# Kernel optimization log

Measured on AMD Instinct MI355X. Metric: run time of the kernel, lower is better.

The kernel has to match this reference:

```python
import jax, jax.numpy as jnp
import numpy as np

PZ = 16          # partition_size
SMOOTH = 1e-8


def setup_inputs() -> dict:
    key = jax.random.key(0)
    k1, k2, k3, k4 = jax.random.split(key, 4)
    shape = (4, 2, 160, 160, 160)  # [N, C, Z, X, Y]
    pred = jax.random.uniform(k1, shape, dtype=jnp.float32)
    groundtruth = jax.random.uniform(k2, shape, dtype=jnp.float32)
    a = jax.random.uniform(k3, (1,), dtype=jnp.float32)
    b = jax.random.uniform(k4, (1,), dtype=jnp.float32)
    return {"pred": pred, "groundtruth": groundtruth, "a": a, "b": b}


def _blocks(t):
    # [N,C,Z,X,Y] -> rows of per-(block, channel) voxels [N*nz*nx*ny*C, PZ^3]
    # matches the torch loops: blocks ordered (N, zz, xx, yy) with channel dim
    # of each block concatenated along dim 0 before flattening dims 1..-1.
    N, C, Z, X, Y = t.shape
    nz, nx, ny = Z // PZ, X // PZ, Y // PZ
    t = t.reshape(N, C, nz, PZ, nx, PZ, ny, PZ)
    t = t.transpose(0, 2, 4, 6, 1, 3, 5, 7)  # [N,nz,nx,ny,C,pz,pz,pz]
    return t.reshape(N * nz * nx * ny * C, PZ * PZ * PZ)


def reference(pred, groundtruth, a, b):
    p = _blocks(pred)
    g = _blocks(groundtruth)
    tp = jnp.sum(g * p, axis=1)
    fn = jnp.sum(g * (1.0 - p), axis=1)
    fp = jnp.sum((1.0 - g) * p, axis=1)
    denom = fp + fn + SMOOTH
    alpha = a + b * ((fp + SMOOTH) / denom)
    beta = a + b * ((fn + SMOOTH) / denom)
    loss = jnp.sum(1.0 - (tp + SMOOTH) / (tp + alpha * fp + beta * fn + SMOOTH))
    return loss
```

## Files before the change

### kernel.cpp

```cpp
#include <hip/hip_runtime.h>

#define SMOOTH 1e-8f

typedef float f32x4 __attribute__((ext_vector_type(4)));

constexpr int NROWS = 8000;
constexpr int WG1   = 3200;

__global__ __launch_bounds__(256, 4)
void partial_kernel(const float* __restrict__ pred,
                    const float* __restrict__ gt,
                    float* __restrict__ wsq)
{
    int wg = blockIdx.x;
    const int q4 = wg & 3;  wg >>= 2;
    const int c  = wg & 1;  wg >>= 1;
    const int xx = wg % 10; wg /= 10;
    const int zz = wg % 10;
    const int n  = wg / 10;

    const int t    = threadIdx.x;
    const int lane = t & 63;
    const int wave = t >> 6;
    const int z    = zz * 16 + q4 * 4 + wave;

    const long pb = ((long)((n * 2 + c) * 160 + z) * 160 + xx * 16) * 40L;

    const f32x4* p4 = reinterpret_cast<const f32x4*>(pred) + pb + lane;
    const f32x4* g4 = reinterpret_cast<const f32x4*>(gt)  + pb + lane;

    f32x4 P[10], G[10];
    #pragma unroll
    for (int k = 0; k < 10; ++k) {
        P[k] = __builtin_nontemporal_load(p4 + k * 64);
        G[k] = __builtin_nontemporal_load(g4 + k * 64);
    }

    float aS[5] = {0, 0, 0, 0, 0};
    float aG[5] = {0, 0, 0, 0, 0};
    float aP[5] = {0, 0, 0, 0, 0};
    #pragma unroll
    for (int k = 0; k < 10; ++k) {
        const int m = k % 5;
        const f32x4 p = P[k], g = G[k];
        aS[m] += (p.x + p.y) + (p.z + p.w);
        aG[m] += (g.x + g.y) + (g.z + g.w);
        aP[m] += p.x * g.x + p.y * g.y + p.z * g.z + p.w * g.w;
    }

    int rr[5];
    #pragma unroll
    for (int m = 0; m < 5; ++m)
        rr[m] = ((lane + 24 * m) % 40) >> 3;

    float bS[5], bG[5], bP[5];
    #pragma unroll
    for (int r = 0; r < 5; ++r) {
        float s = 0.f, g = 0.f, p = 0.f;
        #pragma unroll
        for (int m = 0; m < 5; ++m) {
            const bool hit = (rr[m] == r);
            s += hit ? aS[m] : 0.f;
            g += hit ? aG[m] : 0.f;
            p += hit ? aP[m] : 0.f;
        }
        bS[r] = s; bG[r] = g; bP[r] = p;
    }

    #pragma unroll
    for (int r = 0; r < 5; ++r) {
        #pragma unroll
        for (int d = 0; d < 5; ++d) {
            const int msk = (d < 2) ? (1 << d) : (1 << (d + 1));
            bS[r] += __shfl_xor(bS[r], msk, 64);
            bG[r] += __shfl_xor(bG[r], msk, 64);
            bP[r] += __shfl_xor(bP[r], msk, 64);
        }
    }

    __shared__ float red[4][2][15];
    const int b = (lane >> 2) & 1;
    if ((lane & 59) == 0) {
        #pragma unroll
        for (int r = 0; r < 5; ++r) {
            red[wave][b][r * 3 + 0] = bS[r];
            red[wave][b][r * 3 + 1] = bG[r];
            red[wave][b][r * 3 + 2] = bP[r];
        }
    }
    __syncthreads();

    if (t < 30) {
        const int yy   = t / 3;
        const int comp = t - yy * 3;
        const int bb = yy & 1, r = yy >> 1;
        const float val = red[0][bb][r * 3 + comp] + red[1][bb][r * 3 + comp] +
                          red[2][bb][r * 3 + comp] + red[3][bb][r * 3 + comp];
        const int row = (((n * 10 + zz) * 10 + xx) * 10 + yy) * 2 + c;
        wsq[(row * 4 + q4) * 3 + comp] = val;
    }
}

__global__ __launch_bounds__(1024)
void finalize_kernel(const float* __restrict__ wsq,
                     const float* __restrict__ a_p,
                     const float* __restrict__ b_p,
                     float* __restrict__ out)
{
    const int t = threadIdx.x;
    const float a = a_p[0], b = b_p[0];
    float sum = 0.f;

    for (int r = t; r < NROWS; r += 1024) {
        const float4 w0 = *reinterpret_cast<const float4*>(wsq + r * 12);
        const float4 w1 = *reinterpret_cast<const float4*>(wsq + r * 12 + 4);
        const float4 w2 = *reinterpret_cast<const float4*>(wsq + r * 12 + 8);
        const float SP  = w0.x + w0.w + w1.z + w2.y;
        const float SG  = w0.y + w1.x + w1.w + w2.z;
        const float SGP = w0.z + w1.y + w2.x + w2.w;

        const float tp = SGP;
        const float fn = SG - SGP;
        const float fp = SP - SGP;
        const float denom = fp + fn + SMOOTH;
        const float alpha = a + b * ((fp + SMOOTH) / denom);
        const float beta  = a + b * ((fn + SMOOTH) / denom);
        sum += 1.f - (tp + SMOOTH) / (tp + alpha * fp + beta * fn + SMOOTH);
    }

    #pragma unroll
    for (int d = 32; d > 0; d >>= 1) sum += __shfl_down(sum, d, 64);

    __shared__ float wsum[16];
    if ((t & 63) == 0) wsum[t >> 6] = sum;
    __syncthreads();
    if (t == 0) {
        float tot = 0.f;
        #pragma unroll
        for (int i = 0; i < 16; ++i) tot += wsum[i];
        out[0] = tot;
    }
}

extern "C" void kernel_launch(void* const* d_in, const int* in_sizes, int n_in,
                              void* d_out, int out_size, void* d_ws, size_t ws_size,
                              hipStream_t stream)
{
    const float* pred = (const float*)d_in[0];
    const float* gt   = (const float*)d_in[1];
    const float* a_p  = (const float*)d_in[2];
    const float* b_p  = (const float*)d_in[3];
    float* out = (float*)d_out;
    float* wsq = (float*)d_ws;

    partial_kernel<<<WG1, 256, 0, stream>>>(pred, gt, wsq);
    finalize_kernel<<<1, 1024, 0, stream>>>(wsq, a_p, b_p, out);
}
```

Before: 252.8 us.

## Use single-wave workgroups with double-buffered plane loads and parallel atomic finalize

Each partial-kernel workgroup becomes one 64-lane wave that processes four z-planes in sequence. It uses two register buffers so the loads for the next plane are issued before the current plane is summed, with sched_barriers to keep that order. This drops the cross-wave LDS reduction and gives each wave more loads in flight. The finalize step now runs across many blocks and combines results with atomicAdd, which needs an extra launch to zero the output. The cost is a launch of only 3200 tiny workgroups, higher register pressure from 40 vector registers of buffers, and an extra kernel launch.

```diff
diff --git a/kernel.cpp b/kernel.cpp
--- a/kernel.cpp
+++ b/kernel.cpp
@@ -7,7 +7,9 @@
 constexpr int NROWS = 8000;
 constexpr int WG1   = 3200;
 
-__global__ __launch_bounds__(256, 4)
+__global__ void zero_out_kernel(float* out) { out[0] = 0.0f; }
+
+__global__ __launch_bounds__(64, 2)
 void partial_kernel(const float* __restrict__ pred,
                     const float* __restrict__ gt,
                     float* __restrict__ wsq)
@@ -19,34 +21,49 @@
     const int zz = wg % 10;
     const int n  = wg / 10;
 
-    const int t    = threadIdx.x;
-    const int lane = t & 63;
-    const int wave = t >> 6;
-    const int z    = zz * 16 + q4 * 4 + wave;
+    const int lane = threadIdx.x;
+    const int z0   = zz * 16 + q4 * 4;
 
-    const long pb = ((long)((n * 2 + c) * 160 + z) * 160 + xx * 16) * 40L;
+    const long pb0 = ((long)((n * 2 + c) * 160 + z0) * 160 + xx * 16) * 40L;
+    constexpr long PSTR = 6400;
 
-    const f32x4* p4 = reinterpret_cast<const f32x4*>(pred) + pb + lane;
-    const f32x4* g4 = reinterpret_cast<const f32x4*>(gt)  + pb + lane;
+    const f32x4* p4 = reinterpret_cast<const f32x4*>(pred) + pb0 + lane;
+    const f32x4* g4 = reinterpret_cast<const f32x4*>(gt)  + pb0 + lane;
 
-    f32x4 P[10], G[10];
-    #pragma unroll
-    for (int k = 0; k < 10; ++k) {
-        P[k] = __builtin_nontemporal_load(p4 + k * 64);
-        G[k] = __builtin_nontemporal_load(g4 + k * 64);
+    f32x4 PA[10], GA[10], PB[10], GB[10];
+    float aS[5] = {0,0,0,0,0}, aG[5] = {0,0,0,0,0}, aP[5] = {0,0,0,0,0};
+
+#define ISSUE(Pbuf, Gbuf, plane)                                              \
+    _Pragma("unroll")                                                         \
+    for (int k = 0; k < 10; ++k) {                                            \
+        Pbuf[k] = __builtin_nontemporal_load(p4 + (plane) * PSTR + k * 64);   \
+        Gbuf[k] = __builtin_nontemporal_load(g4 + (plane) * PSTR + k * 64);   \
     }
 
-    float aS[5] = {0, 0, 0, 0, 0};
-    float aG[5] = {0, 0, 0, 0, 0};
-    float aP[5] = {0, 0, 0, 0, 0};
-    #pragma unroll
-    for (int k = 0; k < 10; ++k) {
-        const int m = k % 5;
-        const f32x4 p = P[k], g = G[k];
-        aS[m] += (p.x + p.y) + (p.z + p.w);
-        aG[m] += (g.x + g.y) + (g.z + g.w);
-        aP[m] += p.x * g.x + p.y * g.y + p.z * g.z + p.w * g.w;
+#define CONSUME(Pbuf, Gbuf)                                                   \
+    _Pragma("unroll")                                                         \
+    for (int k = 0; k < 10; ++k) {                                            \
+        const int m = k % 5;                                                  \
+        const f32x4 p = Pbuf[k], g = Gbuf[k];                                 \
+        aS[m] += (p.x + p.y) + (p.z + p.w);                                   \
+        aG[m] += (g.x + g.y) + (g.z + g.w);                                   \
+        aP[m] += p.x * g.x + p.y * g.y + p.z * g.z + p.w * g.w;               \
     }
+
+    ISSUE(PA, GA, 0)
+    __builtin_amdgcn_sched_barrier(0);
+    ISSUE(PB, GB, 1)
+    __builtin_amdgcn_sched_barrier(0);
+    CONSUME(PA, GA)
+    ISSUE(PA, GA, 2)
+    __builtin_amdgcn_sched_barrier(0);
+    CONSUME(PB, GB)
+    ISSUE(PB, GB, 3)
+    __builtin_amdgcn_sched_barrier(0);
+    CONSUME(PA, GA)
+    CONSUME(PB, GB)
+#undef ISSUE
+#undef CONSUME
 
     int rr[5];
     #pragma unroll
@@ -78,40 +95,37 @@
         }
     }
 
-    __shared__ float red[4][2][15];
+    __shared__ float red[2][15];
     const int b = (lane >> 2) & 1;
     if ((lane & 59) == 0) {
         #pragma unroll
         for (int r = 0; r < 5; ++r) {
-            red[wave][b][r * 3 + 0] = bS[r];
-            red[wave][b][r * 3 + 1] = bG[r];
-            red[wave][b][r * 3 + 2] = bP[r];
+            red[b][r * 3 + 0] = bS[r];
+            red[b][r * 3 + 1] = bG[r];
+            red[b][r * 3 + 2] = bP[r];
         }
     }
     __syncthreads();
 
-    if (t < 30) {
-        const int yy   = t / 3;
-        const int comp = t - yy * 3;
+    if (lane < 30) {
+        const int yy   = lane / 3;
+        const int comp = lane - yy * 3;
         const int bb = yy & 1, r = yy >> 1;
-        const float val = red[0][bb][r * 3 + comp] + red[1][bb][r * 3 + comp] +
-                          red[2][bb][r * 3 + comp] + red[3][bb][r * 3 + comp];
+        const float val = red[bb][r * 3 + comp];
         const int row = (((n * 10 + zz) * 10 + xx) * 10 + yy) * 2 + c;
         wsq[(row * 4 + q4) * 3 + comp] = val;
     }
 }
 
-__global__ __launch_bounds__(1024)
+__global__ __launch_bounds__(256)
 void finalize_kernel(const float* __restrict__ wsq,
                      const float* __restrict__ a_p,
                      const float* __restrict__ b_p,
                      float* __restrict__ out)
 {
-    const int t = threadIdx.x;
-    const float a = a_p[0], b = b_p[0];
-    float sum = 0.f;
-
-    for (int r = t; r < NROWS; r += 1024) {
+    const int r = blockIdx.x * 256 + threadIdx.x;
+    float term = 0.f;
+    if (r < NROWS) {
         const float4 w0 = *reinterpret_cast<const float4*>(wsq + r * 12);
         const float4 w1 = *reinterpret_cast<const float4*>(wsq + r * 12 + 4);
         const float4 w2 = *reinterpret_cast<const float4*>(wsq + r * 12 + 8);
@@ -122,24 +136,15 @@
         const float tp = SGP;
         const float fn = SG - SGP;
         const float fp = SP - SGP;
+        const float a = a_p[0], b = b_p[0];
         const float denom = fp + fn + SMOOTH;
         const float alpha = a + b * ((fp + SMOOTH) / denom);
         const float beta  = a + b * ((fn + SMOOTH) / denom);
-        sum += 1.f - (tp + SMOOTH) / (tp + alpha * fp + beta * fn + SMOOTH);
+        term = 1.f - (tp + SMOOTH) / (tp + alpha * fp + beta * fn + SMOOTH);
     }
-
     #pragma unroll
-    for (int d = 32; d > 0; d >>= 1) sum += __shfl_down(sum, d, 64);
-
-    __shared__ float wsum[16];
-    if ((t & 63) == 0) wsum[t >> 6] = sum;
-    __syncthreads();
-    if (t == 0) {
-        float tot = 0.f;
-        #pragma unroll
-        for (int i = 0; i < 16; ++i) tot += wsum[i];
-        out[0] = tot;
-    }
+    for (int d = 32; d > 0; d >>= 1) term += __shfl_down(term, d, 64);
+    if ((threadIdx.x & 63) == 0) atomicAdd(out, term);
 }
 
 extern "C" void kernel_launch(void* const* d_in, const int* in_sizes, int n_in,
@@ -153,6 +158,7 @@
     float* out = (float*)d_out;
     float* wsq = (float*)d_ws;
 
-    partial_kernel<<<WG1, 256, 0, stream>>>(pred, gt, wsq);
-    finalize_kernel<<<1, 1024, 0, stream>>>(wsq, a_p, b_p, out);
+    zero_out_kernel<<<1, 1, 0, stream>>>(out);
+    partial_kernel<<<WG1, 64, 0, stream>>>(pred, gt, wsq);
+    finalize_kernel<<<(NROWS + 255) / 256, 256, 0, stream>>>(wsq, a_p, b_p, out);
 }
```

After: 279.5 us. 1.11x slower.
